# Optimization experiments

Measured on AMD Instinct MI355X. Metric: run time of the kernel, lower is better.

## Reference

```python
import jax, jax.numpy as jnp
import numpy as np

B, S, D = 2, 2048, 1024
H, DH = 16, 64
EPS = 1e-5

def setup_inputs() -> dict:
    key = jax.random.key(0)
    ks = jax.random.split(key, 8)
    s = 0.02
    return {
        "x": jax.random.normal(ks[0], (B, S, D), dtype=jnp.float32),
        "ln_gamma": jnp.ones((D,), jnp.float32),
        "ln_beta": jnp.zeros((D,), jnp.float32),
        "wq": jax.random.normal(ks[1], (D, H * DH), jnp.float32) * s,
        "bq": jnp.zeros((H * DH,), jnp.float32),
        "wk": jax.random.normal(ks[2], (D, H * DH), jnp.float32) * s,
        "bk": jnp.zeros((H * DH,), jnp.float32),
        "wv": jax.random.normal(ks[3], (D, H * DH), jnp.float32) * s,
        "bv": jnp.zeros((H * DH,), jnp.float32),
        "wo": jax.random.normal(ks[4], (H * DH, D), jnp.float32) * s,
        "bo": jnp.zeros((D,), jnp.float32),
    }

def reference(x, ln_gamma, ln_beta, wq, bq, wk, bk, wv, bv, wo, bo):
    # Pre-LayerNorm over d_model
    mu = jnp.mean(x, axis=-1, keepdims=True)
    var = jnp.var(x, axis=-1, keepdims=True)
    xn = (x - mu) * jax.lax.rsqrt(var + EPS) * ln_gamma + ln_beta

    b, s, _ = xn.shape
    q = (xn @ wq + bq).reshape(b, s, H, DH)
    k = (xn @ wk + bk).reshape(b, s, H, DH)
    v = (xn @ wv + bv).reshape(b, s, H, DH)

    scale = jnp.sqrt(jnp.float32(DH))
    scores = jnp.einsum('bihd,bjhd->bhij', q, k) / scale  # [b,h,s,s]
    att = jax.nn.softmax(scores, axis=-1)
    out = jnp.einsum('bhij,bjhd->bihd', att, v).reshape(b, s, H * DH)
    return out @ wo + bo
```

## Files before the change

### kernel.cpp

```cpp
#include <hip/hip_runtime.h>
#include <math.h>

#define SEQ   2048
#define DM    1024
#define NHEAD 16
#define HD    64
#define NTOK  4096
#define EPS   1e-5f
#define SCALE_C 0.18033688f

typedef __attribute__((ext_vector_type(8))) short v8s;
typedef __attribute__((ext_vector_type(4))) float v4f;
typedef unsigned short ushort_t;

#define GLOAD16(g, l) __builtin_amdgcn_global_load_lds( \
    (const __attribute__((address_space(1))) unsigned int*)(g), \
    (__attribute__((address_space(3))) unsigned int*)(l), 16, 0, 0)

__device__ __forceinline__ unsigned short f2bf(float f) {
  union { float f; unsigned u; } v; v.f = f;
  unsigned r = v.u + 0x7FFFu + ((v.u >> 16) & 1u);
  return (unsigned short)(r >> 16);
}

__device__ __forceinline__ unsigned pack2_bf16(float a, float b) {
  union { float f; unsigned u; } ua, ub;
  ua.f = a; ub.f = b;
  return __builtin_amdgcn_perm(ub.u + 0x8000u, ua.u + 0x8000u, 0x07060302u);
}

__global__ __launch_bounds__(256) void ln_kernel(
    const float* __restrict__ x, const float* __restrict__ g,
    const float* __restrict__ be, ushort_t* __restrict__ y) {
  const int row = blockIdx.x;
  const int t = threadIdx.x;
  const float4 v = ((const float4*)(x + (size_t)row * DM))[t];
  float s  = v.x + v.y + v.z + v.w;
  float ss = v.x*v.x + v.y*v.y + v.z*v.z + v.w*v.w;
  #pragma unroll
  for (int off = 32; off > 0; off >>= 1) {
    s  += __shfl_down(s,  off, 64);
    ss += __shfl_down(ss, off, 64);
  }
  __shared__ float red[8];
  __shared__ float mu_s, rs_s;
  const int wid = t >> 6, lane = t & 63;
  if (lane == 0) { red[wid] = s; red[4 + wid] = ss; }
  __syncthreads();
  if (t == 0) {
    const float S  = red[0] + red[1] + red[2] + red[3];
    const float SS = red[4] + red[5] + red[6] + red[7];
    const float mu  = S * (1.0f / DM);
    const float var = SS * (1.0f / DM) - mu * mu;
    mu_s = mu; rs_s = rsqrtf(var + EPS);
  }
  __syncthreads();
  const float mu = mu_s, r = rs_s;
  const float4 gv = ((const float4*)g)[t];
  const float4 bv = ((const float4*)be)[t];
  ushort4 o;
  o.x = f2bf((v.x - mu) * r * gv.x + bv.x);
  o.y = f2bf((v.y - mu) * r * gv.y + bv.y);
  o.z = f2bf((v.z - mu) * r * gv.z + bv.z);
  o.w = f2bf((v.w - mu) * r * gv.w + bv.w);
  *(ushort4*)(y + (size_t)row * DM + t * 4) = o;
}

__global__ __launch_bounds__(256) void wt_kernel(
    const float* __restrict__ w0, const float* __restrict__ w1,
    const float* __restrict__ w2, const float* __restrict__ w3,
    ushort_t* __restrict__ o0, ushort_t* __restrict__ o1,
    ushort_t* __restrict__ o2, ushort_t* __restrict__ o3) {
  const int z = blockIdx.z;
  const float* w = (z==0) ? w0 : (z==1) ? w1 : (z==2) ? w2 : w3;
  ushort_t* o    = (z==0) ? o0 : (z==1) ? o1 : (z==2) ? o2 : o3;
  __shared__ float tile[64][65];
  const int t = threadIdx.x;
  const int n0 = blockIdx.x * 64, k0 = blockIdx.y * 64;
  const int r = t >> 4, c4 = (t & 15) * 4;
  #pragma unroll
  for (int i = 0; i < 4; ++i) {
    const float4 v = *(const float4*)(w + (size_t)(k0 + r + i*16) * DM + n0 + c4);
    tile[r + i*16][c4 + 0] = v.x;
    tile[r + i*16][c4 + 1] = v.y;
    tile[r + i*16][c4 + 2] = v.z;
    tile[r + i*16][c4 + 3] = v.w;
  }
  __syncthreads();
  #pragma unroll
  for (int i = 0; i < 4; ++i) {
    const int n = r + i*16;
    ushort4 o4;
    o4.x = f2bf(tile[c4 + 0][n]);
    o4.y = f2bf(tile[c4 + 1][n]);
    o4.z = f2bf(tile[c4 + 2][n]);
    o4.w = f2bf(tile[c4 + 3][n]);
    *(ushort4*)(o + (size_t)(n0 + n) * DM + k0 + c4) = o4;
  }
}

__device__ __forceinline__ void gemm_main(ushort_t* lsa, ushort_t* lsb,
    const ushort_t* A, const ushort_t* WT, int m0, int n0, v4f acc[4][4]) {
  const int tid = threadIdx.x;
  const int wid = tid >> 6, lane = tid & 63;
  const int mh = (wid & 1) << 6, nh = (wid >> 1) << 6;
  const int r16 = lane & 15, quad = lane >> 4;
  const int srow = lane >> 2, sch = lane & 3;
  for (int k0 = 0; k0 < DM; k0 += 32) {
    __syncthreads();
    #pragma unroll
    for (int j = 0; j < 2; ++j) {
      const int o = wid * 2 + j;
      GLOAD16(A  + (size_t)(m0 + o*16 + srow) * DM + k0 + sch*8, lsa + o*512);
      GLOAD16(WT + (size_t)(n0 + o*16 + srow) * DM + k0 + sch*8, lsb + o*512);
    }
    __syncthreads();
    v8s af[4], bfr[4];
    #pragma unroll
    for (int i = 0; i < 4; ++i) {
      af[i]  = *(const v8s*)(lsa + (mh + i*16 + r16)*32 + quad*8);
      bfr[i] = *(const v8s*)(lsb + (nh + i*16 + r16)*32 + quad*8);
    }
    #pragma unroll
    for (int i = 0; i < 4; ++i)
      #pragma unroll
      for (int j = 0; j < 4; ++j)
        acc[i][j] = __builtin_amdgcn_mfma_f32_16x16x32_bf16(af[i], bfr[j], acc[i][j], 0, 0, 0);
  }
}

__global__ __launch_bounds__(256, 2) void gemm_qkv(const ushort_t* __restrict__ xn,
    const ushort_t* __restrict__ wtq, const ushort_t* __restrict__ wtk, const ushort_t* __restrict__ wtv,
    const float* __restrict__ bq, const float* __restrict__ bk, const float* __restrict__ bv,
    ushort_t* __restrict__ qo, ushort_t* __restrict__ ko, ushort_t* __restrict__ vto) {
  __shared__ ushort_t lsa[128*32];
  __shared__ ushort_t lsb[128*32];
  const int z = blockIdx.z;
  const ushort_t* WT = (z == 0) ? wtq : (z == 1) ? wtk : wtv;
  const float* bias  = (z == 0) ? bq  : (z == 1) ? bk  : bv;
  const int m0 = blockIdx.y * 128, n0 = blockIdx.x * 128;
  v4f acc[4][4];
  #pragma unroll
  for (int i = 0; i < 4; ++i)
    #pragma unroll
    for (int j = 0; j < 4; ++j) acc[i][j] = (v4f){0.f, 0.f, 0.f, 0.f};
  gemm_main(lsa, lsb, xn, WT, m0, n0, acc);
  const int tid = threadIdx.x, wid = tid >> 6, lane = tid & 63;
  const int mh = (wid & 1) << 6, nh = (wid >> 1) << 6;
  const int r16 = lane & 15, quad = lane >> 4;
  if (z < 2) {
    ushort_t* out = (z == 0) ? qo : ko;
    const float sc = (z == 0) ? SCALE_C : 1.0f;
    #pragma unroll
    for (int bn = 0; bn < 4; ++bn) {
      const int col = n0 + nh + bn*16 + r16;
      const float bb = bias[col];
      #pragma unroll
      for (int am = 0; am < 4; ++am) {
        const int tb = m0 + mh + am*16 + quad*4;
        #pragma unroll
        for (int r = 0; r < 4; ++r)
          out[(size_t)(tb + r) * DM + col] = f2bf((acc[am][bn][r] + bb) * sc);
      }
    }
  } else {
    #pragma unroll
    for (int bn = 0; bn < 4; ++bn) {
      const int col = n0 + nh + bn*16 + r16;
      const float bb = bias[col];
      const int h = col >> 6, d = col & 63;
      #pragma unroll
      for (int am = 0; am < 4; ++am) {
        const int tb = m0 + mh + am*16 + quad*4;
        const int b = tb >> 11, t = tb & 2047;
        ushort4 o4;
        o4.x = f2bf(acc[am][bn][0] + bb);
        o4.y = f2bf(acc[am][bn][1] + bb);
        o4.z = f2bf(acc[am][bn][2] + bb);
        o4.w = f2bf(acc[am][bn][3] + bb);
        *(ushort4*)(vto + ((size_t)(b*NHEAD + h) * HD + d) * SEQ + t) = o4;
      }
    }
  }
}

__global__ __launch_bounds__(256, 2) void gemm_out(const ushort_t* __restrict__ A,
    const ushort_t* __restrict__ WT, const float* __restrict__ bias,
    float* __restrict__ out) {
  __shared__ ushort_t lsa[128*32];
  __shared__ ushort_t lsb[64*32];
  const int tid = threadIdx.x, wid = tid >> 6, lane = tid & 63;
  const int mh = (wid & 1) * 64, nh = (wid >> 1) * 32;
  const int r16 = lane & 15, quad = lane >> 4;
  const int srow = lane >> 2, sch = lane & 3;
  const int m0 = blockIdx.y * 128, n0 = blockIdx.x * 64;
  v4f acc[4][2];
  #pragma unroll
  for (int i = 0; i < 4; ++i)
    #pragma unroll
    for (int j = 0; j < 2; ++j) acc[i][j] = (v4f){0.f, 0.f, 0.f, 0.f};
  for (int k0 = 0; k0 < DM; k0 += 32) {
    __syncthreads();
    #pragma unroll
    for (int j = 0; j < 3; ++j) {
      const int o = wid * 3 + j;
      if (o < 8)
        GLOAD16(A  + (size_t)(m0 + o*16 + srow) * DM + k0 + sch*8, lsa + o*512);
      else
        GLOAD16(WT + (size_t)(n0 + (o-8)*16 + srow) * DM + k0 + sch*8, lsb + (o-8)*512);
    }
    __syncthreads();
    v8s af[4], bfr[2];
    #pragma unroll
    for (int i = 0; i < 4; ++i)
      af[i] = *(const v8s*)(lsa + (mh + i*16 + r16)*32 + quad*8);
    #pragma unroll
    for (int j = 0; j < 2; ++j)
      bfr[j] = *(const v8s*)(lsb + (nh + j*16 + r16)*32 + quad*8);
    #pragma unroll
    for (int i = 0; i < 4; ++i)
      #pragma unroll
      for (int j = 0; j < 2; ++j)
        acc[i][j] = __builtin_amdgcn_mfma_f32_16x16x32_bf16(af[i], bfr[j], acc[i][j], 0, 0, 0);
  }
  #pragma unroll
  for (int bn = 0; bn < 2; ++bn) {
    const int col = n0 + nh + bn*16 + r16;
    const float bb = bias[col];
    #pragma unroll
    for (int am = 0; am < 4; ++am) {
      const int tb = m0 + mh + am*16 + quad*4;
      #pragma unroll
      for (int r = 0; r < 4; ++r)
        out[(size_t)(tb + r) * DM + col] = acc[am][bn][r] + bb;
    }
  }
}

#define PROW 72
__global__ __launch_bounds__(256, 4) void attn_kernel(
    const ushort_t* __restrict__ Q, const ushort_t* __restrict__ K,
    const ushort_t* __restrict__ Vt, ushort_t* __restrict__ O) {
  __shared__ ushort_t kbuf[8*512];
  __shared__ ushort_t vbuf[8*512];
  __shared__ ushort_t pbuf[64*PROW];
  __shared__ float    lred[4][64];
  const int tid = threadIdx.x, wid = tid >> 6, lane = tid & 63;
  const int r16 = lane & 15, quad = lane >> 4;
  const int q0 = blockIdx.x * 64, bh = blockIdx.y;
  const int b = bh >> 4, h = bh & 15;
  const ushort_t* gQ = Q + (size_t)b * SEQ * DM + h * HD;
  const ushort_t* gK = K + (size_t)b * SEQ * DM + h * HD;
  const ushort_t* gV = Vt + (size_t)bh * HD * SEQ;

  v8s qfr[4][2];
  #pragma unroll
  for (int qa = 0; qa < 4; ++qa) {
    const ushort_t* p = gQ + (size_t)(q0 + qa*16 + r16) * DM + quad * 8;
    qfr[qa][0] = *(const v8s*)p;
    qfr[qa][1] = *(const v8s*)(p + 32);
  }
  v4f acco[4];
  #pragma unroll
  for (int i = 0; i < 4; ++i) acco[i] = (v4f){0.f, 0.f, 0.f, 0.f};
  float lrun[4] = {0.f, 0.f, 0.f, 0.f};

  for (int kt = 0; kt < SEQ / 64; ++kt) {
    const int k0 = kt * 64;
    __syncthreads();
    if (wid < 2) {
      #pragma unroll
      for (int j = 0; j < 4; ++j) {
        const int o = (wid & 1) * 4 + j;
        GLOAD16(gK + (size_t)(k0 + (o >> 1) * 16 + r16) * DM + (o & 1) * 32 + quad * 8,
                kbuf + o * 512);
      }
    } else {
      #pragma unroll
      for (int j = 0; j < 4; ++j) {
        const int o = (wid & 1) * 4 + j;
        GLOAD16(gV + (size_t)((o & 3) * 16 + r16) * SEQ + k0 + (o >> 2) * 32 + quad * 8,
                vbuf + o * 512);
      }
    }
    __syncthreads();

    const v8s ka0 = *(const v8s*)(kbuf + (wid*2 + 0) * 512 + lane * 8);
    const v8s ka1 = *(const v8s*)(kbuf + (wid*2 + 1) * 512 + lane * 8);
    v4f sacc[4];
    #pragma unroll
    for (int qa = 0; qa < 4; ++qa) {
      sacc[qa] = (v4f){0.f, 0.f, 0.f, 0.f};
      sacc[qa] = __builtin_amdgcn_mfma_f32_16x16x32_bf16(ka0, qfr[qa][0], sacc[qa], 0, 0, 0);
      sacc[qa] = __builtin_amdgcn_mfma_f32_16x16x32_bf16(ka1, qfr[qa][1], sacc[qa], 0, 0, 0);
    }

    #pragma unroll
    for (int qa = 0; qa < 4; ++qa) {
      const float e0 = __builtin_amdgcn_exp2f(sacc[qa][0]);
      const float e1 = __builtin_amdgcn_exp2f(sacc[qa][1]);
      const float e2 = __builtin_amdgcn_exp2f(sacc[qa][2]);
      const float e3 = __builtin_amdgcn_exp2f(sacc[qa][3]);
      float ls = (e0 + e1) + (e2 + e3);
      ls += __shfl_xor(ls, 16, 64);
      ls += __shfl_xor(ls, 32, 64);
      lrun[qa] += ls;
      uint2 d2;
      d2.x = pack2_bf16(e0, e1);
      d2.y = pack2_bf16(e2, e3);
      *(uint2*)(pbuf + (qa*16 + r16) * PROW + wid*16 + quad*4) = d2;
    }

    __syncthreads();

    const v8s vf0 = *(const v8s*)(vbuf + (0*4 + wid) * 512 + lane * 8);
    const v8s vf1 = *(const v8s*)(vbuf + (1*4 + wid) * 512 + lane * 8);
    #pragma unroll
    for (int qa = 0; qa < 4; ++qa) {
      const v8s pb0 = *(const v8s*)(pbuf + (qa*16 + r16) * PROW + quad*8);
      const v8s pb1 = *(const v8s*)(pbuf + (qa*16 + r16) * PROW + 32 + quad*8);
      acco[qa] = __builtin_amdgcn_mfma_f32_16x16x32_bf16(vf0, pb0, acco[qa], 0, 0, 0);
      acco[qa] = __builtin_amdgcn_mfma_f32_16x16x32_bf16(vf1, pb1, acco[qa], 0, 0, 0);
    }
  }

  if (quad == 0) {
    #pragma unroll
    for (int qa = 0; qa < 4; ++qa) lred[wid][qa*16 + r16] = lrun[qa];
  }
  __syncthreads();
  ushort_t* gO = O + (size_t)b * SEQ * DM + h * HD;
  #pragma unroll
  for (int qa = 0; qa < 4; ++qa) {
    const int q = qa*16 + r16;
    const float inv = 1.f / (((lred[0][q] + lred[1][q]) + (lred[2][q] + lred[3][q])));
    ushort4 o4;
    o4.x = f2bf(acco[qa][0] * inv);
    o4.y = f2bf(acco[qa][1] * inv);
    o4.z = f2bf(acco[qa][2] * inv);
    o4.w = f2bf(acco[qa][3] * inv);
    *(ushort4*)(gO + (size_t)(q0 + q) * DM + wid*16 + quad*4) = o4;
  }
}

extern "C" void kernel_launch(void* const* d_in, const int* in_sizes, int n_in,
                              void* d_out, int out_size, void* d_ws, size_t ws_size,
                              hipStream_t stream) {
  const float* x     = (const float*)d_in[0];
  const float* gamma = (const float*)d_in[1];
  const float* beta  = (const float*)d_in[2];
  const float* wq    = (const float*)d_in[3];
  const float* bq    = (const float*)d_in[4];
  const float* wk    = (const float*)d_in[5];
  const float* bk    = (const float*)d_in[6];
  const float* wv    = (const float*)d_in[7];
  const float* bv    = (const float*)d_in[8];
  const float* wo    = (const float*)d_in[9];
  const float* bo    = (const float*)d_in[10];
  float* out = (float*)d_out;

  unsigned char* w8 = (unsigned char*)d_ws;
  const size_t MB = 1024 * 1024;
  ushort_t* xn  = (ushort_t*)(w8 + 0 * MB);
  ushort_t* qb  = (ushort_t*)(w8 + 8 * MB);
  ushort_t* kb  = (ushort_t*)(w8 + 16 * MB);
  ushort_t* vt  = (ushort_t*)(w8 + 24 * MB);
  ushort_t* wtq = (ushort_t*)(w8 + 32 * MB);
  ushort_t* wtk = (ushort_t*)(w8 + 34 * MB);
  ushort_t* wtv = (ushort_t*)(w8 + 36 * MB);
  ushort_t* wto = (ushort_t*)(w8 + 38 * MB);
  ushort_t* ob  = xn;

  ln_kernel<<<dim3(NTOK), dim3(256), 0, stream>>>(x, gamma, beta, xn);
  wt_kernel<<<dim3(16, 16, 4), dim3(256), 0, stream>>>(wq, wk, wv, wo, wtq, wtk, wtv, wto);
  gemm_qkv<<<dim3(8, 32, 3), dim3(256), 0, stream>>>(xn, wtq, wtk, wtv, bq, bk, bv, qb, kb, vt);
  attn_kernel<<<dim3(SEQ / 64, 2 * NHEAD), dim3(256), 0, stream>>>(qb, kb, vt, ob);
  gemm_out<<<dim3(16, 32), dim3(256), 0, stream>>>(ob, wto, bo, out);
}
```

Measured before the change: 222.6 us.

## Double-buffer K/V tiles in attention and enlarge output GEMM tile

The attention kernel now double-buffers its K and V shared-memory tiles, prefetching the next tile while the current one is computed, which cuts one barrier's worth of load latency per iteration. The P buffer is relaid into MFMA-fragment order so reads become contiguous lane*8 loads without padding. The output projection reuses the shared gemm_main helper with a 128x128 tile instead of 128x64, halving the grid and improving operand reuse. The costs are more LDS per block, which may limit occupancy, and fewer blocks for the output GEMM.

```diff
diff --git a/kernel.cpp b/kernel.cpp
--- a/kernel.cpp
+++ b/kernel.cpp
@@ -188,43 +188,19 @@
     const ushort_t* __restrict__ WT, const float* __restrict__ bias,
     float* __restrict__ out) {
   __shared__ ushort_t lsa[128*32];
-  __shared__ ushort_t lsb[64*32];
+  __shared__ ushort_t lsb[128*32];
+  const int m0 = blockIdx.y * 128, n0 = blockIdx.x * 128;
+  v4f acc[4][4];
+  #pragma unroll
+  for (int i = 0; i < 4; ++i)
+    #pragma unroll
+    for (int j = 0; j < 4; ++j) acc[i][j] = (v4f){0.f, 0.f, 0.f, 0.f};
+  gemm_main(lsa, lsb, A, WT, m0, n0, acc);
   const int tid = threadIdx.x, wid = tid >> 6, lane = tid & 63;
-  const int mh = (wid & 1) * 64, nh = (wid >> 1) * 32;
+  const int mh = (wid & 1) << 6, nh = (wid >> 1) << 6;
   const int r16 = lane & 15, quad = lane >> 4;
-  const int srow = lane >> 2, sch = lane & 3;
-  const int m0 = blockIdx.y * 128, n0 = blockIdx.x * 64;
-  v4f acc[4][2];
-  #pragma unroll
-  for (int i = 0; i < 4; ++i)
-    #pragma unroll
-    for (int j = 0; j < 2; ++j) acc[i][j] = (v4f){0.f, 0.f, 0.f, 0.f};
-  for (int k0 = 0; k0 < DM; k0 += 32) {
-    __syncthreads();
-    #pragma unroll
-    for (int j = 0; j < 3; ++j) {
-      const int o = wid * 3 + j;
-      if (o < 8)
-        GLOAD16(A  + (size_t)(m0 + o*16 + srow) * DM + k0 + sch*8, lsa + o*512);
-      else
-        GLOAD16(WT + (size_t)(n0 + (o-8)*16 + srow) * DM + k0 + sch*8, lsb + (o-8)*512);
-    }
-    __syncthreads();
-    v8s af[4], bfr[2];
-    #pragma unroll
-    for (int i = 0; i < 4; ++i)
-      af[i] = *(const v8s*)(lsa + (mh + i*16 + r16)*32 + quad*8);
-    #pragma unroll
-    for (int j = 0; j < 2; ++j)
-      bfr[j] = *(const v8s*)(lsb + (nh + j*16 + r16)*32 + quad*8);
-    #pragma unroll
-    for (int i = 0; i < 4; ++i)
-      #pragma unroll
-      for (int j = 0; j < 2; ++j)
-        acc[i][j] = __builtin_amdgcn_mfma_f32_16x16x32_bf16(af[i], bfr[j], acc[i][j], 0, 0, 0);
-  }
-  #pragma unroll
-  for (int bn = 0; bn < 2; ++bn) {
+  #pragma unroll
+  for (int bn = 0; bn < 4; ++bn) {
     const int col = n0 + nh + bn*16 + r16;
     const float bb = bias[col];
     #pragma unroll
@@ -237,14 +213,12 @@
   }
 }
 
-#define PROW 72
 __global__ __launch_bounds__(256, 4) void attn_kernel(
     const ushort_t* __restrict__ Q, const ushort_t* __restrict__ K,
     const ushort_t* __restrict__ Vt, ushort_t* __restrict__ O) {
-  __shared__ ushort_t kbuf[8*512];
-  __shared__ ushort_t vbuf[8*512];
-  __shared__ ushort_t pbuf[64*PROW];
-  __shared__ float    lred[4][64];
+  __shared__ ushort_t kbuf[2][8*512];
+  __shared__ ushort_t vbuf[2][8*512];
+  __shared__ ushort_t pbuf[8*512];
   const int tid = threadIdx.x, wid = tid >> 6, lane = tid & 63;
   const int r16 = lane & 15, quad = lane >> 4;
   const int q0 = blockIdx.x * 64, bh = blockIdx.y;
@@ -253,6 +227,25 @@
   const ushort_t* gK = K + (size_t)b * SEQ * DM + h * HD;
   const ushort_t* gV = Vt + (size_t)bh * HD * SEQ;
 
+  auto stage = [&](int kt, int buf) {
+    const int k0 = kt * 64;
+    if (wid < 2) {
+      #pragma unroll
+      for (int j = 0; j < 4; ++j) {
+        const int o = (wid & 1) * 4 + j;
+        GLOAD16(gK + (size_t)(k0 + (o >> 1) * 16 + r16) * DM + (o & 1) * 32 + quad * 8,
+                &kbuf[buf][o * 512]);
+      }
+    } else {
+      #pragma unroll
+      for (int j = 0; j < 4; ++j) {
+        const int o = (wid & 1) * 4 + j;
+        GLOAD16(gV + (size_t)((o & 3) * 16 + r16) * SEQ + k0 + (o >> 2) * 32 + quad * 8,
+                &vbuf[buf][o * 512]);
+      }
+    }
+  };
+
   v8s qfr[4][2];
   #pragma unroll
   for (int qa = 0; qa < 4; ++qa) {
@@ -265,28 +258,18 @@
   for (int i = 0; i < 4; ++i) acco[i] = (v4f){0.f, 0.f, 0.f, 0.f};
   float lrun[4] = {0.f, 0.f, 0.f, 0.f};
 
+  const int pwoff = ((wid & 1) * 2 + (quad >> 1)) * 128 + r16 * 8 + (quad & 1) * 4;
+  const int pblk0 = (wid >> 1) * 512;
+
+  stage(0, 0);
+  __syncthreads();
+
   for (int kt = 0; kt < SEQ / 64; ++kt) {
-    const int k0 = kt * 64;
-    __syncthreads();
-    if (wid < 2) {
-      #pragma unroll
-      for (int j = 0; j < 4; ++j) {
-        const int o = (wid & 1) * 4 + j;
-        GLOAD16(gK + (size_t)(k0 + (o >> 1) * 16 + r16) * DM + (o & 1) * 32 + quad * 8,
-                kbuf + o * 512);
-      }
-    } else {
-      #pragma unroll
-      for (int j = 0; j < 4; ++j) {
-        const int o = (wid & 1) * 4 + j;
-        GLOAD16(gV + (size_t)((o & 3) * 16 + r16) * SEQ + k0 + (o >> 2) * 32 + quad * 8,
-                vbuf + o * 512);
-      }
-    }
-    __syncthreads();
-
-    const v8s ka0 = *(const v8s*)(kbuf + (wid*2 + 0) * 512 + lane * 8);
-    const v8s ka1 = *(const v8s*)(kbuf + (wid*2 + 1) * 512 + lane * 8);
+    const int cur = kt & 1, nxt = cur ^ 1;
+    if (kt + 1 < SEQ / 64) stage(kt + 1, nxt);
+
+    const v8s ka0 = *(const v8s*)(&kbuf[cur][(wid*2 + 0) * 512] + lane * 8);
+    const v8s ka1 = *(const v8s*)(&kbuf[cur][(wid*2 + 1) * 512] + lane * 8);
     v4f sacc[4];
     #pragma unroll
     for (int qa = 0; qa < 4; ++qa) {
@@ -308,32 +291,35 @@
       uint2 d2;
       d2.x = pack2_bf16(e0, e1);
       d2.y = pack2_bf16(e2, e3);
-      *(uint2*)(pbuf + (qa*16 + r16) * PROW + wid*16 + quad*4) = d2;
+      *(uint2*)(pbuf + (qa*2) * 512 + pblk0 + pwoff) = d2;
     }
 
     __syncthreads();
 
-    const v8s vf0 = *(const v8s*)(vbuf + (0*4 + wid) * 512 + lane * 8);
-    const v8s vf1 = *(const v8s*)(vbuf + (1*4 + wid) * 512 + lane * 8);
+    const v8s vf0 = *(const v8s*)(&vbuf[cur][(0*4 + wid) * 512] + lane * 8);
+    const v8s vf1 = *(const v8s*)(&vbuf[cur][(1*4 + wid) * 512] + lane * 8);
     #pragma unroll
     for (int qa = 0; qa < 4; ++qa) {
-      const v8s pb0 = *(const v8s*)(pbuf + (qa*16 + r16) * PROW + quad*8);
-      const v8s pb1 = *(const v8s*)(pbuf + (qa*16 + r16) * PROW + 32 + quad*8);
+      const v8s pb0 = *(const v8s*)(pbuf + (qa*2 + 0) * 512 + lane * 8);
+      const v8s pb1 = *(const v8s*)(pbuf + (qa*2 + 1) * 512 + lane * 8);
       acco[qa] = __builtin_amdgcn_mfma_f32_16x16x32_bf16(vf0, pb0, acco[qa], 0, 0, 0);
       acco[qa] = __builtin_amdgcn_mfma_f32_16x16x32_bf16(vf1, pb1, acco[qa], 0, 0, 0);
     }
-  }
-
+
+    __syncthreads();
+  }
+
+  float* lred = (float*)pbuf;
   if (quad == 0) {
     #pragma unroll
-    for (int qa = 0; qa < 4; ++qa) lred[wid][qa*16 + r16] = lrun[qa];
+    for (int qa = 0; qa < 4; ++qa) lred[wid*64 + qa*16 + r16] = lrun[qa];
   }
   __syncthreads();
   ushort_t* gO = O + (size_t)b * SEQ * DM + h * HD;
   #pragma unroll
   for (int qa = 0; qa < 4; ++qa) {
     const int q = qa*16 + r16;
-    const float inv = 1.f / (((lred[0][q] + lred[1][q]) + (lred[2][q] + lred[3][q])));
+    const float inv = 1.f / ((lred[0*64 + q] + lred[1*64 + q]) + (lred[2*64 + q] + lred[3*64 + q]));
     ushort4 o4;
     o4.x = f2bf(acco[qa][0] * inv);
     o4.y = f2bf(acco[qa][1] * inv);
@@ -375,5 +361,5 @@
   wt_kernel<<<dim3(16, 16, 4), dim3(256), 0, stream>>>(wq, wk, wv, wo, wtq, wtk, wtv, wto);
   gemm_qkv<<<dim3(8, 32, 3), dim3(256), 0, stream>>>(xn, wtq, wtk, wtv, bq, bk, bv, qb, kb, vt);
   attn_kernel<<<dim3(SEQ / 64, 2 * NHEAD), dim3(256), 0, stream>>>(qb, kb, vt, ob);
-  gemm_out<<<dim3(16, 32), dim3(256), 0, stream>>>(ob, wto, bo, out);
-}
+  gemm_out<<<dim3(8, 32, 1), dim3(256), 0, stream>>>(ob, wto, bo, out);
+}
```

After: 221.3 us. About the same (-0.6%).
